# Optimization experiments

Measured on AMD Instinct MI355X. Metric: run time of the kernel, lower is better.

## Reference

```python
import jax, jax.numpy as jnp
import numpy as np

B, S, H, F, E, TOPK = 2, 2048, 1024, 2048, 8, 2


def setup_inputs() -> dict:
    key = jax.random.key(0)
    k1, k2, k3, k4, k5 = jax.random.split(key, 5)
    scale_h = 1.0 / np.sqrt(H)
    scale_f = 1.0 / np.sqrt(F)
    return {
        "hidden_states": jax.random.normal(k1, (B, S, H), dtype=jnp.float32),
        "gate_w": jax.random.normal(k2, (E, H), dtype=jnp.float32) * scale_h,
        "w1": jax.random.normal(k3, (E, F, H), dtype=jnp.float32) * scale_h,
        "w2": jax.random.normal(k4, (E, H, F), dtype=jnp.float32) * scale_f,
        "w3": jax.random.normal(k5, (E, F, H), dtype=jnp.float32) * scale_h,
    }


def reference(hidden_states, gate_w, w1, w2, w3):
    b, s, h = hidden_states.shape
    x = hidden_states.reshape(-1, h)                      # [T, H]
    T = x.shape[0]
    router_logits = x @ gate_w.T                          # [T, E]
    probs = jax.nn.softmax(router_logits.astype(jnp.float32), axis=-1)
    rw, sel = jax.lax.top_k(probs, TOPK)                  # [T, k]
    rw = rw / jnp.sum(rw, axis=-1, keepdims=True)
    rw = rw.astype(x.dtype)
    # combine weights [T, E]: routing weight where selected, else 0
    combine = jnp.zeros((T, E), dtype=x.dtype).at[
        jnp.arange(T)[:, None], sel].add(rw)
    # dense dispatch: compute every expert on all tokens, mask via combine
    h1 = jnp.einsum('th,efh->etf', x, w1)                 # [E, T, F]
    h3 = jnp.einsum('th,efh->etf', x, w3)
    gated = jax.nn.silu(h1) * h3
    out_e = jnp.einsum('etf,ehf->eth', gated, w2)         # [E, T, H]
    final = jnp.einsum('eth,te->th', out_e, combine)      # [T, H]
    return final.reshape(b, s, h), router_logits
```

## Files before the change

kernel.cpp:

```cpp
#include <hip/hip_runtime.h>
#include <hip/hip_bf16.h>

#define TT 4096
#define HH 1024
#define FF 2048
#define EE 8
#define NC32 2048

typedef short short8_t __attribute__((ext_vector_type(8)));
typedef float f32x4 __attribute__((ext_vector_type(4)));

__device__ __forceinline__ unsigned short f2b(float f) {
  union { float f; unsigned u; } v; v.f = f;
  return (unsigned short)((v.u + 0x7fffu + ((v.u >> 16) & 1u)) >> 16);
}

__device__ __forceinline__ void gload16(const unsigned short* g, unsigned short* l) {
  __builtin_amdgcn_global_load_lds(
      (const __attribute__((address_space(1))) void*)g,
      (__attribute__((address_space(3))) void*)l, 16, 0, 0);
}

__device__ __forceinline__ void conv_ilp(const float* __restrict__ src,
                                         unsigned short* __restrict__ dst,
                                         int c, int tid) {
  size_t base = (size_t)c * 8192 + tid * 4;
  float4 v[8];
#pragma unroll
  for (int j = 0; j < 8; ++j)
    v[j] = *reinterpret_cast<const float4*>(src + base + j * 1024);
#pragma unroll
  for (int j = 0; j < 8; ++j) {
    ushort4 b4;
    b4.x = f2b(v[j].x); b4.y = f2b(v[j].y); b4.z = f2b(v[j].z); b4.w = f2b(v[j].w);
    *reinterpret_cast<ushort4*>(dst + base + j * 1024) = b4;
  }
}

__global__ __launch_bounds__(256) void front_kernel(
    const float* __restrict__ x, const float* __restrict__ gw,
    const float* __restrict__ w1, const float* __restrict__ w3,
    const float* __restrict__ w2,
    float* __restrict__ out_logits, float* __restrict__ final_out,
    unsigned short* __restrict__ xbf,
    unsigned short* __restrict__ w1bf, unsigned short* __restrict__ w3bf,
    unsigned short* __restrict__ w2bf,
    int* __restrict__ sel01, float2* __restrict__ w01)
{
  int tid = threadIdx.x;
  int b = blockIdx.x;
  if (b >= TT) {
    int cb = b - TT;
    if (cb < NC32)          conv_ilp(w1, w1bf, cb, tid);
    else if (cb < 2 * NC32) conv_ilp(w3, w3bf, cb - NC32, tid);
    else                    conv_ilp(w2, w2bf, cb - 2 * NC32, tid);
    return;
  }
  int t = b;

  __shared__ float xs[HH];
  __shared__ float lg[EE];

  float4 v = reinterpret_cast<const float4*>(x + (size_t)t * HH)[tid];
  xs[tid * 4 + 0] = v.x; xs[tid * 4 + 1] = v.y;
  xs[tid * 4 + 2] = v.z; xs[tid * 4 + 3] = v.w;
  ushort4 b4;
  b4.x = f2b(v.x); b4.y = f2b(v.y); b4.z = f2b(v.z); b4.w = f2b(v.w);
  reinterpret_cast<ushort4*>(xbf + (size_t)t * HH)[tid] = b4;
  float4 z4; z4.x = z4.y = z4.z = z4.w = 0.f;
  reinterpret_cast<float4*>(final_out + (size_t)t * HH)[tid] = z4;
  __syncthreads();

  int lane = tid & 63, wv = tid >> 6;
  for (int e = wv; e < EE; e += 4) {
    float s = 0.f;
    const float* g = gw + (size_t)e * HH;
#pragma unroll
    for (int j = 0; j < HH / 64; ++j) s += xs[lane + j * 64] * g[lane + j * 64];
#pragma unroll
    for (int off = 32; off > 0; off >>= 1) s += __shfl_down(s, off);
    if (lane == 0) lg[e] = s;
  }
  __syncthreads();

  if (tid < 8) out_logits[(size_t)t * EE + tid] = lg[tid];
  if (tid == 0) {
    float l[EE];
#pragma unroll
    for (int e = 0; e < EE; ++e) l[e] = lg[e];
    int e0 = 0;
#pragma unroll
    for (int e = 1; e < EE; ++e) if (l[e] > l[e0]) e0 = e;
    int e1 = -1;
#pragma unroll
    for (int e = 0; e < EE; ++e) if (e != e0 && (e1 < 0 || l[e] > l[e1])) e1 = e;
    float p1 = expf(l[e1] - l[e0]);
    float w0 = 1.f / (1.f + p1);
    float w1v = p1 * w0;
    sel01[t] = e0 | (e1 << 8);
    w01[t] = make_float2(w0, w1v);
  }
}

__global__ __launch_bounds__(256) void build_kernel(
    const int* __restrict__ sel01, const float2* __restrict__ w01,
    int* __restrict__ counts, int* __restrict__ tokidx, float* __restrict__ rww)
{
  int e = blockIdx.x;
  int tid = threadIdx.x, lane = tid & 63, wv = tid >> 6;
  __shared__ int wsum[4];
  int base = 0;
  for (int t0 = 0; t0 < TT; t0 += 256) {
    int t = t0 + tid;
    int s = sel01[t];
    int e0 = s & 255, e1 = (s >> 8) & 255;
    bool hit = (e0 == e) || (e1 == e);
    float w = 0.f;
    if (hit) { float2 ww = w01[t]; w = (e0 == e) ? ww.x : ww.y; }
    unsigned long long m = __ballot(hit);
    int wpre = __popcll(m & ((1ull << lane) - 1));
    if (lane == 63) wsum[wv] = wpre + (hit ? 1 : 0);
    __syncthreads();
    int wbase = base;
    for (int q = 0; q < wv; ++q) wbase += wsum[q];
    if (hit) {
      int pos = wbase + wpre;
      tokidx[e * TT + pos] = t;
      rww[e * TT + pos] = w;
    }
    base += wsum[0] + wsum[1] + wsum[2] + wsum[3];
    __syncthreads();
  }
  if (tid == 0) counts[e] = base;
}

__global__ __launch_bounds__(256) void conv_kernel(
    const float* __restrict__ src, unsigned short* __restrict__ dst)
{
  conv_ilp(src, dst, blockIdx.x, threadIdx.x);
}

__global__ __launch_bounds__(256) void up_gate_kernel(
    const unsigned short* __restrict__ xbf,
    const unsigned short* __restrict__ w1bf, const unsigned short* __restrict__ w3bf,
    const int* __restrict__ counts, const int* __restrict__ tokidx,
    unsigned short* __restrict__ gated)
{
  int e = blockIdx.z;
  int n = counts[e];
  int row0 = blockIdx.y * 128;
  if (row0 >= n) return;
  int fbase = blockIdx.x * 64;

  int pe = 0;
  for (int q = 0; q < e; ++q) pe += (counts[q] + 127) & ~127;

  __shared__ unsigned short As[2][128 * 32];
  __shared__ unsigned short B1s[2][64 * 32];
  __shared__ unsigned short B3s[2][64 * 32];

  int tid = threadIdx.x;
  int lane = tid & 63, wv = tid >> 6;
  int srow = wv * 16 + (lane >> 2);
  int skoff = (lane & 3) * 8;

  int r0 = min(row0 + srow, n - 1);
  int r1 = min(row0 + 64 + srow, n - 1);
  int t0 = tokidx[e * TT + r0];
  int t1 = tokidx[e * TT + r1];
  const unsigned short* ga0 = xbf + (size_t)t0 * HH + skoff;
  const unsigned short* ga1 = xbf + (size_t)t1 * HH + skoff;
  const unsigned short* gb1 = w1bf + ((size_t)e * FF + fbase + srow) * HH + skoff;
  const unsigned short* gb3 = w3bf + ((size_t)e * FF + fbase + srow) * HH + skoff;

  int wr = (wv >> 1) * 64, wc = (wv & 1) * 32;
  int fr = lane & 15, fk = (lane >> 4) * 8;

  f32x4 acc1[4][2], acc3[4][2];
#pragma unroll
  for (int m = 0; m < 4; ++m)
#pragma unroll
    for (int nn = 0; nn < 2; ++nn) { acc1[m][nn] = (f32x4)0.f; acc3[m][nn] = (f32x4)0.f; }

  gload16(ga0, &As[0][wv * 512]);
  gload16(ga1, &As[0][2048 + wv * 512]);
  gload16(gb1, &B1s[0][wv * 512]);
  gload16(gb3, &B3s[0][wv * 512]);

  int cur = 0;
  for (int k0 = 0; k0 < HH; k0 += 32) {
    __syncthreads();
    if (k0 + 32 < HH) {
      int nxt = cur ^ 1, kn = k0 + 32;
      gload16(ga0 + kn, &As[nxt][wv * 512]);
      gload16(ga1 + kn, &As[nxt][2048 + wv * 512]);
      gload16(gb1 + kn, &B1s[nxt][wv * 512]);
      gload16(gb3 + kn, &B3s[nxt][wv * 512]);
    }

    short8_t a[4], b1f[2], b3f[2];
#pragma unroll
    for (int m = 0; m < 4; ++m)
      a[m] = *reinterpret_cast<const short8_t*>(&As[cur][(wr + m * 16 + fr) * 32 + fk]);
#pragma unroll
    for (int nn = 0; nn < 2; ++nn) {
      b1f[nn] = *reinterpret_cast<const short8_t*>(&B1s[cur][(wc + nn * 16 + fr) * 32 + fk]);
      b3f[nn] = *reinterpret_cast<const short8_t*>(&B3s[cur][(wc + nn * 16 + fr) * 32 + fk]);
    }
#pragma unroll
    for (int m = 0; m < 4; ++m)
#pragma unroll
      for (int nn = 0; nn < 2; ++nn) {
        acc1[m][nn] = __builtin_amdgcn_mfma_f32_16x16x32_bf16(a[m], b1f[nn], acc1[m][nn], 0, 0, 0);
        acc3[m][nn] = __builtin_amdgcn_mfma_f32_16x16x32_bf16(a[m], b3f[nn], acc3[m][nn], 0, 0, 0);
      }
    cur ^= 1;
  }

  size_t gbase = ((size_t)pe + row0) * FF + fbase;
#pragma unroll
  for (int m = 0; m < 4; ++m) {
#pragma unroll
    for (int nn = 0; nn < 2; ++nn) {
      f32x4 h1v = acc1[m][nn], h3v = acc3[m][nn];
#pragma unroll
      for (int j = 0; j < 4; ++j) {
        float z = h1v[j];
        float val = (z / (1.f + expf(-z))) * h3v[j];
        int r = wr + m * 16 + (lane >> 4) * 4 + j;
        int c = wc + nn * 16 + fr;
        gated[gbase + (size_t)r * FF + c] = f2b(val);
      }
    }
  }
}

__global__ __launch_bounds__(256) void down_kernel(
    const unsigned short* __restrict__ gated,
    const unsigned short* __restrict__ w2bf,
    const int* __restrict__ counts, const int* __restrict__ tokidx,
    const float* __restrict__ rww,
    float* __restrict__ final_out)
{
  int e = blockIdx.z;
  int n = counts[e];
  int row0 = blockIdx.y * 128;
  if (row0 >= n) return;
  int hbase = blockIdx.x * 128;
  int valid = min(128, n - row0);

  int pe = 0;
  for (int q = 0; q < e; ++q) pe += (counts[q] + 127) & ~127;

  __shared__ unsigned short As[2][128 * 32];
  __shared__ unsigned short Bs[2][128 * 32];

  int tid = threadIdx.x;
  int lane = tid & 63, wv = tid >> 6;
  int srow = wv * 16 + (lane >> 2);
  int skoff = (lane & 3) * 8;

  const unsigned short* ga0 = gated + ((size_t)pe + row0 + srow) * FF + skoff;
  const unsigned short* ga1 = ga0 + (size_t)64 * FF;
  const unsigned short* gb0 = w2bf + ((size_t)e * HH + hbase + srow) * FF + skoff;
  const unsigned short* gb1 = gb0 + (size_t)64 * FF;

  int wr = (wv >> 1) * 64, wc = (wv & 1) * 64;
  int fr = lane & 15, fk = (lane >> 4) * 8;

  f32x4 acc[4][4];
#pragma unroll
  for (int m = 0; m < 4; ++m)
#pragma unroll
    for (int nn = 0; nn < 4; ++nn) acc[m][nn] = (f32x4)0.f;

  gload16(ga0, &As[0][wv * 512]);
  gload16(ga1, &As[0][2048 + wv * 512]);
  gload16(gb0, &Bs[0][wv * 512]);
  gload16(gb1, &Bs[0][2048 + wv * 512]);

  int cur = 0;
  for (int k0 = 0; k0 < FF; k0 += 32) {
    __syncthreads();
    if (k0 + 32 < FF) {
      int nxt = cur ^ 1, kn = k0 + 32;
      gload16(ga0 + kn, &As[nxt][wv * 512]);
      gload16(ga1 + kn, &As[nxt][2048 + wv * 512]);
      gload16(gb0 + kn, &Bs[nxt][wv * 512]);
      gload16(gb1 + kn, &Bs[nxt][2048 + wv * 512]);
    }

    short8_t a[4], bf[4];
#pragma unroll
    for (int m = 0; m < 4; ++m)
      a[m] = *reinterpret_cast<const short8_t*>(&As[cur][(wr + m * 16 + fr) * 32 + fk]);
#pragma unroll
    for (int nn = 0; nn < 4; ++nn)
      bf[nn] = *reinterpret_cast<const short8_t*>(&Bs[cur][(wc + nn * 16 + fr) * 32 + fk]);
#pragma unroll
    for (int m = 0; m < 4; ++m)
#pragma unroll
      for (int nn = 0; nn < 4; ++nn)
        acc[m][nn] = __builtin_amdgcn_mfma_f32_16x16x32_bf16(a[m], bf[nn], acc[m][nn], 0, 0, 0);
    cur ^= 1;
  }

#pragma unroll
  for (int m = 0; m < 4; ++m) {
    int rbase = wr + m * 16 + (lane >> 4) * 4;
#pragma unroll
    for (int j = 0; j < 4; ++j) {
      int r = rbase + j;
      if (r < valid) {
        int t = tokidx[e * TT + row0 + r];
        float w = rww[e * TT + row0 + r];
#pragma unroll
        for (int nn = 0; nn < 4; ++nn) {
          int c = hbase + wc + nn * 16 + fr;
          atomicAdd(&final_out[(size_t)t * HH + c], w * acc[m][nn][j]);
        }
      }
    }
  }
}

extern "C" void kernel_launch(void* const* d_in, const int* in_sizes, int n_in,
                              void* d_out, int out_size, void* d_ws, size_t ws_size,
                              hipStream_t stream) {
  const float* x  = (const float*)d_in[0];
  const float* gw = (const float*)d_in[1];
  const float* w1 = (const float*)d_in[2];
  const float* w2 = (const float*)d_in[3];
  const float* w3 = (const float*)d_in[4];

  float* final_out  = (float*)d_out;
  float* out_logits = final_out + (size_t)TT * HH;

  char* ws = (char*)d_ws;
  int*    counts = (int*)(ws + 0);
  int*    sel01  = (int*)(ws + 1024);
  float2* w01    = (float2*)(ws + 20480);
  int*    tokidx = (int*)(ws + 53248);
  float*  rww    = (float*)(ws + 184320);
  unsigned short* xbf   = (unsigned short*)(ws + 315392);
  unsigned short* w1bf  = (unsigned short*)(ws + 8704000);
  unsigned short* w3bf  = (unsigned short*)(ws + 42258432);
  unsigned short* gated = (unsigned short*)(ws + 75812864);
  const size_t base_end = 113561600;
  bool big = ws_size >= base_end + 33554432;
  unsigned short* w2bf = big ? (unsigned short*)(ws + base_end) : w1bf;

  int nconvblk = (big ? 3 : 2) * NC32;
  front_kernel<<<TT + nconvblk, 256, 0, stream>>>(
      x, gw, w1, w3, w2, out_logits, final_out, xbf, w1bf, w3bf, w2bf,
      sel01, w01);
  build_kernel<<<EE, 256, 0, stream>>>(sel01, w01, counts, tokidx, rww);
  up_gate_kernel<<<dim3(FF / 64, TT / 128, EE), 256, 0, stream>>>(
      xbf, w1bf, w3bf, counts, tokidx, gated);
  if (!big) conv_kernel<<<NC32, 256, 0, stream>>>(w2, w1bf);
  down_kernel<<<dim3(HH / 128, TT / 128, EE), 256, 0, stream>>>(
      gated, w2bf, counts, tokidx, rww, final_out);
}
```

Measured before the change: 266.2 us.

## Deepen K tiles to 64 with XOR-swizzled LDS and explicit vmcnt pipelining

```diff
diff --git a/kernel.cpp b/kernel.cpp
--- a/kernel.cpp
+++ b/kernel.cpp
@@ -6,6 +6,7 @@
 #define FF 2048
 #define EE 8
 #define NC32 2048
+#define LDSU 32768
 
 typedef short short8_t __attribute__((ext_vector_type(8)));
 typedef float f32x4 __attribute__((ext_vector_type(4)));
@@ -15,11 +16,13 @@
   return (unsigned short)((v.u + 0x7fffu + ((v.u >> 16) & 1u)) >> 16);
 }
 
-__device__ __forceinline__ void gload16(const unsigned short* g, unsigned short* l) {
+__device__ __forceinline__ void gload16(const unsigned short* g, void* l) {
   __builtin_amdgcn_global_load_lds(
       (const __attribute__((address_space(1))) void*)g,
       (__attribute__((address_space(3))) void*)l, 16, 0, 0);
 }
+
+#define FENCE asm volatile("" ::: "memory")
 
 __device__ __forceinline__ void conv_ilp(const float* __restrict__ src,
                                          unsigned short* __restrict__ dst,
@@ -155,26 +158,29 @@
   int pe = 0;
   for (int q = 0; q < e; ++q) pe += (counts[q] + 127) & ~127;
 
-  __shared__ unsigned short As[2][128 * 32];
-  __shared__ unsigned short B1s[2][64 * 32];
-  __shared__ unsigned short B3s[2][64 * 32];
+  __shared__ __align__(16) char lds[2 * LDSU];
 
   int tid = threadIdx.x;
   int lane = tid & 63, wv = tid >> 6;
-  int srow = wv * 16 + (lane >> 2);
-  int skoff = (lane & 3) * 8;
-
-  int r0 = min(row0 + srow, n - 1);
-  int r1 = min(row0 + 64 + srow, n - 1);
-  int t0 = tokidx[e * TT + r0];
-  int t1 = tokidx[e * TT + r1];
-  const unsigned short* ga0 = xbf + (size_t)t0 * HH + skoff;
-  const unsigned short* ga1 = xbf + (size_t)t1 * HH + skoff;
-  const unsigned short* gb1 = w1bf + ((size_t)e * FF + fbase + srow) * HH + skoff;
-  const unsigned short* gb3 = w3bf + ((size_t)e * FF + fbase + srow) * HH + skoff;
+  int sb = (tid & 7) ^ ((tid >> 3) & 7);
+
+  const unsigned short* ga[4];
+#pragma unroll
+  for (int j = 0; j < 4; ++j) {
+    int r = min(row0 + (tid >> 3) + 32 * j, n - 1);
+    ga[j] = xbf + (size_t)tokidx[e * TT + r] * HH + sb * 8;
+  }
+  const unsigned short* gb1[2];
+  const unsigned short* gb3[2];
+#pragma unroll
+  for (int j = 0; j < 2; ++j) {
+    size_t rw_ = (size_t)e * FF + fbase + (tid >> 3) + 32 * j;
+    gb1[j] = w1bf + rw_ * HH + sb * 8;
+    gb3[j] = w3bf + rw_ * HH + sb * 8;
+  }
 
   int wr = (wv >> 1) * 64, wc = (wv & 1) * 32;
-  int fr = lane & 15, fk = (lane >> 4) * 8;
+  int fr = lane & 15, kq = lane >> 4, l7 = lane & 7;
 
   f32x4 acc1[4][2], acc3[4][2];
 #pragma unroll
@@ -182,40 +188,46 @@
 #pragma unroll
     for (int nn = 0; nn < 2; ++nn) { acc1[m][nn] = (f32x4)0.f; acc3[m][nn] = (f32x4)0.f; }
 
-  gload16(ga0, &As[0][wv * 512]);
-  gload16(ga1, &As[0][2048 + wv * 512]);
-  gload16(gb1, &B1s[0][wv * 512]);
-  gload16(gb3, &B3s[0][wv * 512]);
-
-  int cur = 0;
-  for (int k0 = 0; k0 < HH; k0 += 32) {
-    __syncthreads();
-    if (k0 + 32 < HH) {
-      int nxt = cur ^ 1, kn = k0 + 32;
-      gload16(ga0 + kn, &As[nxt][wv * 512]);
-      gload16(ga1 + kn, &As[nxt][2048 + wv * 512]);
-      gload16(gb1 + kn, &B1s[nxt][wv * 512]);
-      gload16(gb3 + kn, &B3s[nxt][wv * 512]);
-    }
-
-    short8_t a[4], b1f[2], b3f[2];
-#pragma unroll
-    for (int m = 0; m < 4; ++m)
-      a[m] = *reinterpret_cast<const short8_t*>(&As[cur][(wr + m * 16 + fr) * 32 + fk]);
-#pragma unroll
-    for (int nn = 0; nn < 2; ++nn) {
-      b1f[nn] = *reinterpret_cast<const short8_t*>(&B1s[cur][(wc + nn * 16 + fr) * 32 + fk]);
-      b3f[nn] = *reinterpret_cast<const short8_t*>(&B3s[cur][(wc + nn * 16 + fr) * 32 + fk]);
-    }
-#pragma unroll
-    for (int m = 0; m < 4; ++m)
-#pragma unroll
-      for (int nn = 0; nn < 2; ++nn) {
-        acc1[m][nn] = __builtin_amdgcn_mfma_f32_16x16x32_bf16(a[m], b1f[nn], acc1[m][nn], 0, 0, 0);
-        acc3[m][nn] = __builtin_amdgcn_mfma_f32_16x16x32_bf16(a[m], b3f[nn], acc3[m][nn], 0, 0, 0);
-      }
-    cur ^= 1;
-  }
+#define UG_STAGE(T, SOFF) do {                                                     \
+    _Pragma("unroll") for (int j = 0; j < 4; ++j)                                  \
+      gload16(ga[j] + (T) * 64, lds + (SOFF) + j * 4096 + wv * 1024);              \
+    _Pragma("unroll") for (int j = 0; j < 2; ++j) {                                \
+      gload16(gb1[j] + (T) * 64, lds + (SOFF) + 16384 + j * 4096 + wv * 1024);     \
+      gload16(gb3[j] + (T) * 64, lds + (SOFF) + 24576 + j * 4096 + wv * 1024);     \
+    } } while (0)
+
+#define UG_COMPUTE(SOFF) do {                                                               \
+    _Pragma("unroll") for (int ks = 0; ks < 2; ++ks) {                                      \
+      int bswz = ((ks * 4 + kq) ^ l7) * 16;                                                 \
+      short8_t a[4], b1f[2], b3f[2];                                                        \
+      _Pragma("unroll") for (int m = 0; m < 4; ++m)                                         \
+        a[m] = *(const short8_t*)(lds + (SOFF) + (wr + m * 16 + fr) * 128 + bswz);          \
+      _Pragma("unroll") for (int nn = 0; nn < 2; ++nn) {                                    \
+        b1f[nn] = *(const short8_t*)(lds + (SOFF) + 16384 + (wc + nn * 16 + fr) * 128 + bswz); \
+        b3f[nn] = *(const short8_t*)(lds + (SOFF) + 24576 + (wc + nn * 16 + fr) * 128 + bswz); \
+      }                                                                                     \
+      _Pragma("unroll") for (int m = 0; m < 4; ++m)                                         \
+        _Pragma("unroll") for (int nn = 0; nn < 2; ++nn) {                                  \
+          acc1[m][nn] = __builtin_amdgcn_mfma_f32_16x16x32_bf16(a[m], b1f[nn], acc1[m][nn], 0, 0, 0); \
+          acc3[m][nn] = __builtin_amdgcn_mfma_f32_16x16x32_bf16(a[m], b3f[nn], acc3[m][nn], 0, 0, 0); \
+        } } } while (0)
+
+#define UG_NT 16
+#define UG_ITER(T, SOFF) do {                                          \
+    if ((T) < UG_NT - 1) asm volatile("s_waitcnt vmcnt(8)" ::: "memory"); \
+    else                 asm volatile("s_waitcnt vmcnt(0)" ::: "memory"); \
+    __builtin_amdgcn_s_barrier(); FENCE;                               \
+    UG_COMPUTE(SOFF);                                                  \
+    FENCE; __builtin_amdgcn_s_barrier(); FENCE;                        \
+    if ((T) + 2 < UG_NT) UG_STAGE((T) + 2, SOFF);                      \
+  } while (0)
+
+  UG_STAGE(0, 0);
+  UG_STAGE(1, LDSU);
+  for (int t2 = 0; t2 < UG_NT; t2 += 2) { UG_ITER(t2, 0); UG_ITER(t2 + 1, LDSU); }
+#undef UG_STAGE
+#undef UG_COMPUTE
+#undef UG_ITER
 
   size_t gbase = ((size_t)pe + row0) * FF + fbase;
 #pragma unroll
@@ -252,21 +264,22 @@
   int pe = 0;
   for (int q = 0; q < e; ++q) pe += (counts[q] + 127) & ~127;
 
-  __shared__ unsigned short As[2][128 * 32];
-  __shared__ unsigned short Bs[2][128 * 32];
+  __shared__ __align__(16) char lds[2 * LDSU];
 
   int tid = threadIdx.x;
   int lane = tid & 63, wv = tid >> 6;
-  int srow = wv * 16 + (lane >> 2);
-  int skoff = (lane & 3) * 8;
-
-  const unsigned short* ga0 = gated + ((size_t)pe + row0 + srow) * FF + skoff;
-  const unsigned short* ga1 = ga0 + (size_t)64 * FF;
-  const unsigned short* gb0 = w2bf + ((size_t)e * HH + hbase + srow) * FF + skoff;
-  const unsigned short* gb1 = gb0 + (size_t)64 * FF;
+  int sb = (tid & 7) ^ ((tid >> 3) & 7);
+
+  const unsigned short* ga[4];
+  const unsigned short* gb[4];
+#pragma unroll
+  for (int j = 0; j < 4; ++j) {
+    ga[j] = gated + ((size_t)pe + row0 + (tid >> 3) + 32 * j) * FF + sb * 8;
+    gb[j] = w2bf + ((size_t)e * HH + hbase + (tid >> 3) + 32 * j) * FF + sb * 8;
+  }
 
   int wr = (wv >> 1) * 64, wc = (wv & 1) * 64;
-  int fr = lane & 15, fk = (lane >> 4) * 8;
+  int fr = lane & 15, kq = lane >> 4, l7 = lane & 7;
 
   f32x4 acc[4][4];
 #pragma unroll
@@ -274,36 +287,41 @@
 #pragma unroll
     for (int nn = 0; nn < 4; ++nn) acc[m][nn] = (f32x4)0.f;
 
-  gload16(ga0, &As[0][wv * 512]);
-  gload16(ga1, &As[0][2048 + wv * 512]);
-  gload16(gb0, &Bs[0][wv * 512]);
-  gload16(gb1, &Bs[0][2048 + wv * 512]);
-
-  int cur = 0;
-  for (int k0 = 0; k0 < FF; k0 += 32) {
-    __syncthreads();
-    if (k0 + 32 < FF) {
-      int nxt = cur ^ 1, kn = k0 + 32;
-      gload16(ga0 + kn, &As[nxt][wv * 512]);
-      gload16(ga1 + kn, &As[nxt][2048 + wv * 512]);
-      gload16(gb0 + kn, &Bs[nxt][wv * 512]);
-      gload16(gb1 + kn, &Bs[nxt][2048 + wv * 512]);
-    }
-
-    short8_t a[4], bf[4];
-#pragma unroll
-    for (int m = 0; m < 4; ++m)
-      a[m] = *reinterpret_cast<const short8_t*>(&As[cur][(wr + m * 16 + fr) * 32 + fk]);
-#pragma unroll
-    for (int nn = 0; nn < 4; ++nn)
-      bf[nn] = *reinterpret_cast<const short8_t*>(&Bs[cur][(wc + nn * 16 + fr) * 32 + fk]);
-#pragma unroll
-    for (int m = 0; m < 4; ++m)
-#pragma unroll
-      for (int nn = 0; nn < 4; ++nn)
-        acc[m][nn] = __builtin_amdgcn_mfma_f32_16x16x32_bf16(a[m], bf[nn], acc[m][nn], 0, 0, 0);
-    cur ^= 1;
-  }
+#define DN_STAGE(T, SOFF) do {                                                   \
+    _Pragma("unroll") for (int j = 0; j < 4; ++j) {                              \
+      gload16(ga[j] + (T) * 64, lds + (SOFF) + j * 4096 + wv * 1024);            \
+      gload16(gb[j] + (T) * 64, lds + (SOFF) + 16384 + j * 4096 + wv * 1024);    \
+    } } while (0)
+
+#define DN_COMPUTE(SOFF) do {                                                              \
+    _Pragma("unroll") for (int ks = 0; ks < 2; ++ks) {                                     \
+      int bswz = ((ks * 4 + kq) ^ l7) * 16;                                                \
+      short8_t a[4], bf[4];                                                                \
+      _Pragma("unroll") for (int m = 0; m < 4; ++m)                                        \
+        a[m] = *(const short8_t*)(lds + (SOFF) + (wr + m * 16 + fr) * 128 + bswz);         \
+      _Pragma("unroll") for (int nn = 0; nn < 4; ++nn)                                     \
+        bf[nn] = *(const short8_t*)(lds + (SOFF) + 16384 + (wc + nn * 16 + fr) * 128 + bswz); \
+      _Pragma("unroll") for (int m = 0; m < 4; ++m)                                        \
+        _Pragma("unroll") for (int nn = 0; nn < 4; ++nn)                                   \
+          acc[m][nn] = __builtin_amdgcn_mfma_f32_16x16x32_bf16(a[m], bf[nn], acc[m][nn], 0, 0, 0); \
+    } } while (0)
+
+#define DN_NT 32
+#define DN_ITER(T, SOFF) do {                                          \
+    if ((T) < DN_NT - 1) asm volatile("s_waitcnt vmcnt(8)" ::: "memory"); \
+    else                 asm volatile("s_waitcnt vmcnt(0)" ::: "memory"); \
+    __builtin_amdgcn_s_barrier(); FENCE;                               \
+    DN_COMPUTE(SOFF);                                                  \
+    FENCE; __builtin_amdgcn_s_barrier(); FENCE;                        \
+    if ((T) + 2 < DN_NT) DN_STAGE((T) + 2, SOFF);                      \
+  } while (0)
+
+  DN_STAGE(0, 0);
+  DN_STAGE(1, LDSU);
+  for (int t2 = 0; t2 < DN_NT; t2 += 2) { DN_ITER(t2, 0); DN_ITER(t2 + 1, LDSU); }
+#undef DN_STAGE
+#undef DN_COMPUTE
+#undef DN_ITER
 
 #pragma unroll
   for (int m = 0; m < 4; ++m) {
```

After: 258.6 us. 2.8% less time.

## Enlarge MoE GEMM tiles, swizzle LDS layout, and pipeline loads with explicit waitcnt

Applied to the files above, without the earlier changes.

```diff
diff --git a/kernel.cpp b/kernel.cpp
--- a/kernel.cpp
+++ b/kernel.cpp
@@ -6,6 +6,7 @@
 #define FF 2048
 #define EE 8
 #define NC32 2048
+#define SLOT 24576
 
 typedef short short8_t __attribute__((ext_vector_type(8)));
 typedef float f32x4 __attribute__((ext_vector_type(4)));
@@ -15,11 +16,13 @@
   return (unsigned short)((v.u + 0x7fffu + ((v.u >> 16) & 1u)) >> 16);
 }
 
-__device__ __forceinline__ void gload16(const unsigned short* g, unsigned short* l) {
+__device__ __forceinline__ void gload16(const unsigned short* g, void* l) {
   __builtin_amdgcn_global_load_lds(
       (const __attribute__((address_space(1))) void*)g,
       (__attribute__((address_space(3))) void*)l, 16, 0, 0);
 }
+
+#define FENCE asm volatile("" ::: "memory")
 
 __device__ __forceinline__ void conv_ilp(const float* __restrict__ src,
                                          unsigned short* __restrict__ dst,
@@ -150,84 +153,96 @@
   int n = counts[e];
   int row0 = blockIdx.y * 128;
   if (row0 >= n) return;
-  int fbase = blockIdx.x * 64;
+  int fbase = blockIdx.x * 128;
 
   int pe = 0;
   for (int q = 0; q < e; ++q) pe += (counts[q] + 127) & ~127;
 
-  __shared__ unsigned short As[2][128 * 32];
-  __shared__ unsigned short B1s[2][64 * 32];
-  __shared__ unsigned short B3s[2][64 * 32];
+  __shared__ __align__(16) char lds[2 * SLOT];
 
   int tid = threadIdx.x;
   int lane = tid & 63, wv = tid >> 6;
-  int srow = wv * 16 + (lane >> 2);
-  int skoff = (lane & 3) * 8;
-
-  int r0 = min(row0 + srow, n - 1);
-  int r1 = min(row0 + 64 + srow, n - 1);
-  int t0 = tokidx[e * TT + r0];
-  int t1 = tokidx[e * TT + r1];
-  const unsigned short* ga0 = xbf + (size_t)t0 * HH + skoff;
-  const unsigned short* ga1 = xbf + (size_t)t1 * HH + skoff;
-  const unsigned short* gb1 = w1bf + ((size_t)e * FF + fbase + srow) * HH + skoff;
-  const unsigned short* gb3 = w3bf + ((size_t)e * FF + fbase + srow) * HH + skoff;
-
-  int wr = (wv >> 1) * 64, wc = (wv & 1) * 32;
-  int fr = lane & 15, fk = (lane >> 4) * 8;
-
-  f32x4 acc1[4][2], acc3[4][2];
+  int sr = tid >> 2;
+  int sb = (tid & 3) ^ ((tid >> 3) & 3);
+
+  int r0 = min(row0 + sr, n - 1);
+  int r1 = min(row0 + 64 + sr, n - 1);
+  const unsigned short* ga0 = xbf + (size_t)tokidx[e * TT + r0] * HH + sb * 8;
+  const unsigned short* ga1 = xbf + (size_t)tokidx[e * TT + r1] * HH + sb * 8;
+  const unsigned short* gb1a = w1bf + ((size_t)e * FF + fbase + sr) * HH + sb * 8;
+  const unsigned short* gb1b = gb1a + (size_t)64 * HH;
+  const unsigned short* gb3a = w3bf + ((size_t)e * FF + fbase + sr) * HH + sb * 8;
+  const unsigned short* gb3b = gb3a + (size_t)64 * HH;
+
+  int wr = (wv >> 1) * 64, wc = (wv & 1) * 64;
+  int fr = lane & 15, kq = lane >> 4;
+
+  int offA[4], offB[4];
+#pragma unroll
+  for (int m = 0; m < 4; ++m) {
+    int r = wr + m * 16 + fr;
+    offA[m] = r * 64 + ((kq ^ ((r >> 1) & 3)) << 4);
+  }
+#pragma unroll
+  for (int nn = 0; nn < 4; ++nn) {
+    int r = wc + nn * 16 + fr;
+    offB[nn] = r * 64 + ((kq ^ ((r >> 1) & 3)) << 4);
+  }
+
+  f32x4 acc1[4][4], acc3[4][4];
 #pragma unroll
   for (int m = 0; m < 4; ++m)
 #pragma unroll
-    for (int nn = 0; nn < 2; ++nn) { acc1[m][nn] = (f32x4)0.f; acc3[m][nn] = (f32x4)0.f; }
-
-  gload16(ga0, &As[0][wv * 512]);
-  gload16(ga1, &As[0][2048 + wv * 512]);
-  gload16(gb1, &B1s[0][wv * 512]);
-  gload16(gb3, &B3s[0][wv * 512]);
-
-  int cur = 0;
-  for (int k0 = 0; k0 < HH; k0 += 32) {
-    __syncthreads();
-    if (k0 + 32 < HH) {
-      int nxt = cur ^ 1, kn = k0 + 32;
-      gload16(ga0 + kn, &As[nxt][wv * 512]);
-      gload16(ga1 + kn, &As[nxt][2048 + wv * 512]);
-      gload16(gb1 + kn, &B1s[nxt][wv * 512]);
-      gload16(gb3 + kn, &B3s[nxt][wv * 512]);
-    }
-
-    short8_t a[4], b1f[2], b3f[2];
-#pragma unroll
-    for (int m = 0; m < 4; ++m)
-      a[m] = *reinterpret_cast<const short8_t*>(&As[cur][(wr + m * 16 + fr) * 32 + fk]);
-#pragma unroll
-    for (int nn = 0; nn < 2; ++nn) {
-      b1f[nn] = *reinterpret_cast<const short8_t*>(&B1s[cur][(wc + nn * 16 + fr) * 32 + fk]);
-      b3f[nn] = *reinterpret_cast<const short8_t*>(&B3s[cur][(wc + nn * 16 + fr) * 32 + fk]);
-    }
-#pragma unroll
-    for (int m = 0; m < 4; ++m)
-#pragma unroll
-      for (int nn = 0; nn < 2; ++nn) {
-        acc1[m][nn] = __builtin_amdgcn_mfma_f32_16x16x32_bf16(a[m], b1f[nn], acc1[m][nn], 0, 0, 0);
-        acc3[m][nn] = __builtin_amdgcn_mfma_f32_16x16x32_bf16(a[m], b3f[nn], acc3[m][nn], 0, 0, 0);
-      }
-    cur ^= 1;
-  }
+    for (int nn = 0; nn < 4; ++nn) { acc1[m][nn] = (f32x4)0.f; acc3[m][nn] = (f32x4)0.f; }
+
+#define UG_STAGE(T, SOFF) do {                                  \
+    gload16(ga0  + (T) * 32, lds + (SOFF) +         wv * 1024); \
+    gload16(ga1  + (T) * 32, lds + (SOFF) +  4096 + wv * 1024); \
+    gload16(gb1a + (T) * 32, lds + (SOFF) +  8192 + wv * 1024); \
+    gload16(gb1b + (T) * 32, lds + (SOFF) + 12288 + wv * 1024); \
+    gload16(gb3a + (T) * 32, lds + (SOFF) + 16384 + wv * 1024); \
+    gload16(gb3b + (T) * 32, lds + (SOFF) + 20480 + wv * 1024); } while (0)
+
+#define UG_NT 32
+#define UG_ITER(T, SOFF) do {                                                      \
+    if ((T) < UG_NT - 1) asm volatile("s_waitcnt vmcnt(6)" ::: "memory");          \
+    else                 asm volatile("s_waitcnt vmcnt(0)" ::: "memory");          \
+    __builtin_amdgcn_s_barrier(); FENCE;                                           \
+    short8_t a_[4], b1_[4], b3_[4];                                                \
+    _Pragma("unroll") for (int m = 0; m < 4; ++m)                                  \
+      a_[m] = *(const short8_t*)(lds + (SOFF) + offA[m]);                          \
+    _Pragma("unroll") for (int nn = 0; nn < 4; ++nn) {                             \
+      b1_[nn] = *(const short8_t*)(lds + (SOFF) +  8192 + offB[nn]);               \
+      b3_[nn] = *(const short8_t*)(lds + (SOFF) + 16384 + offB[nn]);               \
+    }                                                                              \
+    __builtin_amdgcn_s_setprio(1);                                                 \
+    _Pragma("unroll") for (int m = 0; m < 4; ++m)                                  \
+      _Pragma("unroll") for (int nn = 0; nn < 4; ++nn) {                           \
+        acc1[m][nn] = __builtin_amdgcn_mfma_f32_16x16x32_bf16(a_[m], b1_[nn], acc1[m][nn], 0, 0, 0); \
+        acc3[m][nn] = __builtin_amdgcn_mfma_f32_16x16x32_bf16(a_[m], b3_[nn], acc3[m][nn], 0, 0, 0); \
+      }                                                                            \
+    __builtin_amdgcn_s_setprio(0);                                                 \
+    FENCE; __builtin_amdgcn_s_barrier(); FENCE;                                    \
+    if ((T) + 2 < UG_NT) UG_STAGE((T) + 2, SOFF);                                  \
+  } while (0)
+
+  UG_STAGE(0, 0);
+  UG_STAGE(1, SLOT);
+  for (int t2 = 0; t2 < UG_NT; t2 += 2) { UG_ITER(t2, 0); UG_ITER(t2 + 1, SLOT); }
+#undef UG_STAGE
+#undef UG_ITER
 
   size_t gbase = ((size_t)pe + row0) * FF + fbase;
 #pragma unroll
   for (int m = 0; m < 4; ++m) {
 #pragma unroll
-    for (int nn = 0; nn < 2; ++nn) {
+    for (int nn = 0; nn < 4; ++nn) {
       f32x4 h1v = acc1[m][nn], h3v = acc3[m][nn];
 #pragma unroll
       for (int j = 0; j < 4; ++j) {
         float z = h1v[j];
         float val = (z / (1.f + expf(-z))) * h3v[j];
-        int r = wr + m * 16 + (lane >> 4) * 4 + j;
+        int r = wr + m * 16 + kq * 4 + j;
         int c = wc + nn * 16 + fr;
         gated[gbase + (size_t)r * FF + c] = f2b(val);
       }
@@ -246,68 +261,83 @@
   int n = counts[e];
   int row0 = blockIdx.y * 128;
   if (row0 >= n) return;
-  int hbase = blockIdx.x * 128;
+  int hbase = blockIdx.x * 256;
   int valid = min(128, n - row0);
 
   int pe = 0;
   for (int q = 0; q < e; ++q) pe += (counts[q] + 127) & ~127;
 
-  __shared__ unsigned short As[2][128 * 32];
-  __shared__ unsigned short Bs[2][128 * 32];
+  __shared__ __align__(16) char lds[2 * SLOT];
 
   int tid = threadIdx.x;
   int lane = tid & 63, wv = tid >> 6;
-  int srow = wv * 16 + (lane >> 2);
-  int skoff = (lane & 3) * 8;
-
-  const unsigned short* ga0 = gated + ((size_t)pe + row0 + srow) * FF + skoff;
+  int sr = tid >> 2;
+  int sb = (tid & 3) ^ ((tid >> 3) & 3);
+
+  const unsigned short* ga0 = gated + ((size_t)pe + row0 + sr) * FF + sb * 8;
   const unsigned short* ga1 = ga0 + (size_t)64 * FF;
-  const unsigned short* gb0 = w2bf + ((size_t)e * HH + hbase + srow) * FF + skoff;
-  const unsigned short* gb1 = gb0 + (size_t)64 * FF;
-
-  int wr = (wv >> 1) * 64, wc = (wv & 1) * 64;
-  int fr = lane & 15, fk = (lane >> 4) * 8;
-
-  f32x4 acc[4][4];
+  const unsigned short* gb0 = w2bf + ((size_t)e * HH + hbase + sr) * FF + sb * 8;
+  const unsigned short* gb1_ = gb0 + (size_t)64 * FF;
+  const unsigned short* gb2_ = gb0 + (size_t)128 * FF;
+  const unsigned short* gb3_ = gb0 + (size_t)192 * FF;
+
+  int wr = (wv >> 1) * 64, wc = (wv & 1) * 128;
+  int fr = lane & 15, kq = lane >> 4;
+
+  int offA[4], offB[8];
+#pragma unroll
+  for (int m = 0; m < 4; ++m) {
+    int r = wr + m * 16 + fr;
+    offA[m] = r * 64 + ((kq ^ ((r >> 1) & 3)) << 4);
+  }
+#pragma unroll
+  for (int nn = 0; nn < 8; ++nn) {
+    int r = wc + nn * 16 + fr;
+    offB[nn] = r * 64 + ((kq ^ ((r >> 1) & 3)) << 4);
+  }
+
+  f32x4 acc[4][8];
 #pragma unroll
   for (int m = 0; m < 4; ++m)
 #pragma unroll
-    for (int nn = 0; nn < 4; ++nn) acc[m][nn] = (f32x4)0.f;
-
-  gload16(ga0, &As[0][wv * 512]);
-  gload16(ga1, &As[0][2048 + wv * 512]);
-  gload16(gb0, &Bs[0][wv * 512]);
-  gload16(gb1, &Bs[0][2048 + wv * 512]);
-
-  int cur = 0;
-  for (int k0 = 0; k0 < FF; k0 += 32) {
-    __syncthreads();
-    if (k0 + 32 < FF) {
-      int nxt = cur ^ 1, kn = k0 + 32;
-      gload16(ga0 + kn, &As[nxt][wv * 512]);
-      gload16(ga1 + kn, &As[nxt][2048 + wv * 512]);
-      gload16(gb0 + kn, &Bs[nxt][wv * 512]);
-      gload16(gb1 + kn, &Bs[nxt][2048 + wv * 512]);
-    }
-
-    short8_t a[4], bf[4];
-#pragma unroll
-    for (int m = 0; m < 4; ++m)
-      a[m] = *reinterpret_cast<const short8_t*>(&As[cur][(wr + m * 16 + fr) * 32 + fk]);
-#pragma unroll
-    for (int nn = 0; nn < 4; ++nn)
-      bf[nn] = *reinterpret_cast<const short8_t*>(&Bs[cur][(wc + nn * 16 + fr) * 32 + fk]);
-#pragma unroll
-    for (int m = 0; m < 4; ++m)
-#pragma unroll
-      for (int nn = 0; nn < 4; ++nn)
-        acc[m][nn] = __builtin_amdgcn_mfma_f32_16x16x32_bf16(a[m], bf[nn], acc[m][nn], 0, 0, 0);
-    cur ^= 1;
-  }
+    for (int nn = 0; nn < 8; ++nn) acc[m][nn] = (f32x4)0.f;
+
+#define DN_STAGE(T, SOFF) do {                                  \
+    gload16(ga0  + (T) * 32, lds + (SOFF) +         wv * 1024); \
+    gload16(ga1  + (T) * 32, lds + (SOFF) +  4096 + wv * 1024); \
+    gload16(gb0  + (T) * 32, lds + (SOFF) +  8192 + wv * 1024); \
+    gload16(gb1_ + (T) * 32, lds + (SOFF) + 12288 + wv * 1024); \
+    gload16(gb2_ + (T) * 32, lds + (SOFF) + 16384 + wv * 1024); \
+    gload16(gb3_ + (T) * 32, lds + (SOFF) + 20480 + wv * 1024); } while (0)
+
+#define DN_NT 64
+#define DN_ITER(T, SOFF) do {                                                      \
+    if ((T) < DN_NT - 1) asm volatile("s_waitcnt vmcnt(6)" ::: "memory");          \
+    else                 asm volatile("s_waitcnt vmcnt(0)" ::: "memory");          \
+    __builtin_amdgcn_s_barrier(); FENCE;                                           \
+    short8_t a_[4], b_[8];                                                         \
+    _Pragma("unroll") for (int m = 0; m < 4; ++m)                                  \
+      a_[m] = *(const short8_t*)(lds + (SOFF) + offA[m]);                          \
+    _Pragma("unroll") for (int nn = 0; nn < 8; ++nn)                               \
+      b_[nn] = *(const short8_t*)(lds + (SOFF) + 8192 + offB[nn]);                 \
+    __builtin_amdgcn_s_setprio(1);                                                 \
+    _Pragma("unroll") for (int m = 0; m < 4; ++m)                                  \
+      _Pragma("unroll") for (int nn = 0; nn < 8; ++nn)                             \
+        acc[m][nn] = __builtin_amdgcn_mfma_f32_16x16x32_bf16(a_[m], b_[nn], acc[m][nn], 0, 0, 0); \
+    __builtin_amdgcn_s_setprio(0);                                                 \
+    FENCE; __builtin_amdgcn_s_barrier(); FENCE;                                    \
+    if ((T) + 2 < DN_NT) DN_STAGE((T) + 2, SOFF);                                  \
+  } while (0)
+
+  DN_STAGE(0, 0);
+  DN_STAGE(1, SLOT);
+  for (int t2 = 0; t2 < DN_NT; t2 += 2) { DN_ITER(t2, 0); DN_ITER(t2 + 1, SLOT); }
+#undef DN_STAGE
+#undef DN_ITER
 
 #pragma unroll
   for (int m = 0; m < 4; ++m) {
-    int rbase = wr + m * 16 + (lane >> 4) * 4;
+    int rbase = wr + m * 16 + kq * 4;
 #pragma unroll
     for (int j = 0; j < 4; ++j) {
       int r = rbase + j;
@@ -315,7 +345,7 @@
         int t = tokidx[e * TT + row0 + r];
         float w = rww[e * TT + row0 + r];
 #pragma unroll
-        for (int nn = 0; nn < 4; ++nn) {
+        for (int nn = 0; nn < 8; ++nn) {
           int c = hbase + wc + nn * 16 + fr;
           atomicAdd(&final_out[(size_t)t * HH + c], w * acc[m][nn][j]);
         }
@@ -355,9 +385,9 @@
       x, gw, w1, w3, w2, out_logits, final_out, xbf, w1bf, w3bf, w2bf,
       sel01, w01);
   build_kernel<<<EE, 256, 0, stream>>>(sel01, w01, counts, tokidx, rww);
-  up_gate_kernel<<<dim3(FF / 64, TT / 128, EE), 256, 0, stream>>>(
+  up_gate_kernel<<<dim3(FF / 128, TT / 128, EE), 256, 0, stream>>>(
       xbf, w1bf, w3bf, counts, tokidx, gated);
   if (!big) conv_kernel<<<NC32, 256, 0, stream>>>(w2, w1bf);
-  down_kernel<<<dim3(HH / 128, TT / 128, EE), 256, 0, stream>>>(
+  down_kernel<<<dim3(HH / 256, TT / 128, EE), 256, 0, stream>>>(
       gated, w2bf, counts, tokidx, rww, final_out);
 }
```

New measurement: 326.5 us. +22.7%, slower.
